# Kernel tuning notes

Measured on AMD Instinct MI355X. Metric: run time of the kernel, lower is better.

The kernel has to match this reference:

```python
import jax, jax.numpy as jnp
import numpy as np

NUM_TAGS = 32
START_ID = 29
STOP_ID = 30
PAD_ID = 31
VOCAB = 50000
EMB = 256
HID = 512          # bidirectional total; per-direction hidden = HID // 2
HD = HID // 2
B = 64
T = 512


def setup_inputs() -> dict:
    key = jax.random.key(0)
    ks = jax.random.split(key, 14)
    # pack_padded_sequence requires sorted-descending lengths; padding at the end
    lengths = np.sort(np.asarray(jax.random.randint(ks[0], (B,), T // 2, T + 1)))[::-1].copy()
    mask = (np.arange(T)[None, :] < lengths[:, None]).astype(np.int32)
    inp = jax.random.randint(ks[1], (B, T), 0, VOCAB, dtype=jnp.int32)
    gold = jax.random.randint(ks[2], (B, T), 0, START_ID, dtype=jnp.int32)  # real tags only
    s = 1.0 / np.sqrt(HD)
    emb = jax.random.normal(ks[3], (VOCAB, EMB), jnp.float32)
    Wih_f = jax.random.uniform(ks[4], (4 * HD, EMB), jnp.float32, -s, s)
    Whh_f = jax.random.uniform(ks[5], (4 * HD, HD), jnp.float32, -s, s)
    b_f = jax.random.uniform(ks[6], (4 * HD,), jnp.float32, -s, s)      # b_ih + b_hh combined
    Wih_b = jax.random.uniform(ks[7], (4 * HD, EMB), jnp.float32, -s, s)
    Whh_b = jax.random.uniform(ks[8], (4 * HD, HD), jnp.float32, -s, s)
    b_b = jax.random.uniform(ks[9], (4 * HD,), jnp.float32, -s, s)
    sl = 1.0 / np.sqrt(HID)
    W_tag = jax.random.uniform(ks[10], (NUM_TAGS, HID), jnp.float32, -sl, sl)
    b_tag = jax.random.uniform(ks[11], (NUM_TAGS,), jnp.float32, -sl, sl)
    trans = np.asarray(jax.random.normal(ks[12], (NUM_TAGS, NUM_TAGS), jnp.float32)).copy()
    # CRF.__init__ constraints
    trans[START_ID, :] = -10000.0
    trans[:, STOP_ID] = -10000.0
    trans[:, PAD_ID] = -10000.0
    trans[PAD_ID, :] = -10000.0
    trans[PAD_ID, STOP_ID] = 0.0
    trans[PAD_ID, PAD_ID] = 0.0
    return dict(inp=inp, gold=gold, mask=jnp.asarray(mask), emb=emb,
                Wih_f=Wih_f, Whh_f=Whh_f, b_f=b_f,
                Wih_b=Wih_b, Whh_b=Whh_b, b_b=b_b,
                W_tag=W_tag, b_tag=b_tag, trans=jnp.asarray(trans))


def _lstm_dir(xW, m, Whh):
    """xW: [T,B,4H] precomputed input projection + bias; m: [T,B,1] float mask; Whh: [4H,H].
    Masked state update replicates packed-sequence behavior (padding at sequence end)."""
    Bb, H = xW.shape[1], Whh.shape[1]

    def step(carry, xm):
        h, c = carry
        x_t, m_t = xm
        g = x_t + h @ Whh.T
        i, f, gg, o = jnp.split(g, 4, axis=-1)  # torch gate order i,f,g,o
        c_new = jax.nn.sigmoid(f) * c + jax.nn.sigmoid(i) * jnp.tanh(gg)
        h_new = jax.nn.sigmoid(o) * jnp.tanh(c_new)
        c = m_t * c_new + (1.0 - m_t) * c
        h = m_t * h_new + (1.0 - m_t) * h
        return (h, c), h

    init = (jnp.zeros((Bb, H), xW.dtype), jnp.zeros((Bb, H), xW.dtype))
    _, hs = jax.lax.scan(step, init, (xW, m))
    return hs  # [T,B,H]


def _forward(inp, gold, mask, emb, Wih_f, Whh_f, b_f, Wih_b, Whh_b, b_b, W_tag, b_tag, trans):
    maskf = mask.astype(jnp.float32)          # [B,T]
    x = emb[inp]                               # [B,T,E]
    xT = jnp.swapaxes(x, 0, 1)                 # [T,B,E]
    mT = maskf.T[:, :, None]                   # [T,B,1]
    h_f = _lstm_dir(xT @ Wih_f.T + b_f, mT, Whh_f)                 # forward direction
    h_b = _lstm_dir((xT @ Wih_b.T + b_b)[::-1], mT[::-1], Whh_b)[::-1]  # backward direction
    h = jnp.concatenate([h_f, h_b], axis=-1)   # [T,B,HID]
    h_tag = (h @ W_tag.T + b_tag) * mT         # masked emissions, [T,B,K]

    K = trans.shape[0]
    Bb = h_tag.shape[1]
    score0 = jnp.full((Bb, K), -10000.0, jnp.float32).at[:, STOP_ID].set(0.0)

    def crf_step(score, em):
        emit_t, m_t = em  # [B,K], [B,1]
        # logsumexp over previous tag j of score[b,j] + emit[b,i] + trans[i,j]
        s = jax.nn.logsumexp(score[:, None, :] + emit_t[:, :, None] + trans[None], axis=-1)
        return m_t * s + (1.0 - m_t) * score, None

    scoreZ, _ = jax.lax.scan(crf_step, score0, (h_tag, mT))
    Z = jax.nn.logsumexp(scoreZ + trans[STOP_ID], axis=-1)  # [B]

    # gold path score (vectorized version of CRF.score)
    h_bt = jnp.swapaxes(h_tag, 0, 1)                          # [B,T,K]
    emit = jnp.take_along_axis(h_bt[:, :-1, :], gold[:, 1:, None].astype(jnp.int32), axis=2)[..., 0]
    tr = trans[gold[:, 1:], gold[:, :-1]]                     # [B,T-1]
    gscore = jnp.sum((emit + tr) * maskf[:, :-1], axis=1)
    lengths = maskf.sum(1).astype(jnp.int32)
    last_tag = jnp.take_along_axis(gold, (lengths - 1)[:, None], axis=1)[:, 0]
    gscore = gscore + trans[STOP_ID, last_tag]
    return Z - gscore  # [B]


def reference(inp, gold, mask, emb, Wih_f, Whh_f, b_f, Wih_b, Whh_b, b_b, W_tag, b_tag, trans):
    return _forward(inp, gold, mask, emb, Wih_f, Whh_f, b_f, Wih_b, Whh_b, b_b, W_tag, b_tag, trans)
```

## Files before the change

### kernel.cpp

```cpp
#include <hip/hip_runtime.h>
#include <stdint.h>

#define T_LEN 512
#define NB 64
#define STOPID 30
#define PADID 31

typedef unsigned short u16;
typedef unsigned int u32;
typedef long long i64;
typedef short bf8 __attribute__((ext_vector_type(8)));
typedef float f32x4 __attribute__((ext_vector_type(4)));
typedef int v4i __attribute__((ext_vector_type(4)));

__device__ __forceinline__ float bf2f(u16 v){ return __uint_as_float(((u32)v) << 16); }
__device__ __forceinline__ u16 f2bf(float f){
  u32 u = __float_as_uint(f);
  return (u16)((u + 0x7FFFu + ((u >> 16) & 1u)) >> 16);
}
__device__ __forceinline__ float sigm(float x){
  return __builtin_amdgcn_rcpf(1.0f + __expf(-x));
}
__device__ __forceinline__ float tanhfast(float x){
  return 1.0f - 2.0f*__builtin_amdgcn_rcpf(1.0f + __expf(2.0f*x));
}
__device__ __forceinline__ v4i mk4(i64 a, i64 b){
  union { i64 q[2]; v4i v; } u; u.q[0]=a; u.q[1]=b; return u.v;
}

#define WSCALE 2032.0f
#define HSCALE 127.0f

extern "C" __global__ __launch_bounds__(256) void kg_emb(
    const int* __restrict__ inp, const float* __restrict__ emb,
    const int* __restrict__ mask,
    const float* __restrict__ whf, const float* __restrict__ whb,
    const float* __restrict__ wif, const float* __restrict__ wib,
    const float* __restrict__ wtag,
    u16* __restrict__ xemb, int* __restrict__ lenv,
    u32* __restrict__ whh8, u16* __restrict__ wih_bf, u16* __restrict__ wtag_bf)
{
  int r = blockIdx.x*2 + (threadIdx.x >> 7);
  int col = (threadIdx.x & 127) * 2;
  int b = r & 63, t = r >> 6;
  int tok = inp[b*T_LEN + t];
  float2 v = *(const float2*)(emb + (size_t)tok*256 + col);
  u32 pk = ((u32)f2bf(v.x)) | (((u32)f2bf(v.y)) << 16);
  *(u32*)(xemb + (size_t)r*256 + col) = pk;

  if (blockIdx.x < 1024) {
    int i = blockIdx.x * 256 + threadIdx.x;
    wih_bf[i]          = f2bf(wif[i]);
    wih_bf[262144 + i] = f2bf(wib[i]);
    if (i < 16384) wtag_bf[i] = f2bf(wtag[i]);
    if (i < 131072) {
      const float* src = (i < 65536) ? (whf + (size_t)i*4) : (whb + (size_t)(i - 65536)*4);
      float4 w4 = *(const float4*)src;
      int b0 = (int)rintf(fminf(fmaxf(w4.x*WSCALE, -127.f), 127.f));
      int b1 = (int)rintf(fminf(fmaxf(w4.y*WSCALE, -127.f), 127.f));
      int b2 = (int)rintf(fminf(fmaxf(w4.z*WSCALE, -127.f), 127.f));
      int b3 = (int)rintf(fminf(fmaxf(w4.w*WSCALE, -127.f), 127.f));
      whh8[i] = (u32)(b0 & 0xFF) | ((u32)(b1 & 0xFF) << 8)
              | ((u32)(b2 & 0xFF) << 16) | ((u32)(b3 & 0xFF) << 24);
    }
  }
  if (blockIdx.x == 0 && threadIdx.x < 64) {
    const int* mrow = mask + threadIdx.x * T_LEN;
    int lo = 256, hi = 512;
    while (lo < hi) { int mid = (lo + hi) >> 1; if (mrow[mid]) lo = mid + 1; else hi = mid; }
    lenv[threadIdx.x] = lo;
  }
}

extern "C" __global__ __launch_bounds__(256, 1) void k1_proj(
    const u16* __restrict__ xemb, const u16* __restrict__ wih,
    const float* __restrict__ b_f, const float* __restrict__ b_b,
    u16* __restrict__ xW)
{
  int tc = blockIdx.x;
  int gb = blockIdx.y;
  int dir  = gb >> 4;
  int nblk = gb & 15;
  int w    = threadIdx.x >> 6;
  int lane = threadIdx.x & 63;
  int lr = lane & 15, q = lane >> 4;

  bf8 bw[4][8];
  const u16* wbase = wih + (size_t)dir*262144 + (size_t)nblk*64*256;
  #pragma unroll
  for (int n = 0; n < 4; ++n)
    #pragma unroll
    for (int kt = 0; kt < 8; ++kt)
      bw[n][kt] = *(const bf8*)(wbase + (size_t)(n*16 + lr)*256 + kt*32 + q*8);
  #pragma unroll
  for (int n = 0; n < 4; ++n) {
    asm volatile("" : "+a"(bw[n][0]), "+a"(bw[n][1]), "+a"(bw[n][2]), "+a"(bw[n][3]));
    asm volatile("" : "+a"(bw[n][4]), "+a"(bw[n][5]), "+a"(bw[n][6]), "+a"(bw[n][7]));
  }

  const float* bias = dir ? b_b : b_f;
  float4 bv[4];
  #pragma unroll
  for (int n = 0; n < 4; ++n) bv[n] = *(const float4*)(bias + nblk*64 + n*16 + q*4);

  for (int ti = 0; ti < 8; ++ti) {
    int t = tc*8 + ti;
    bf8 af[8];
    #pragma unroll
    for (int kt = 0; kt < 8; ++kt)
      af[kt] = *(const bf8*)(xemb + ((size_t)t*64 + w*16 + lr)*256 + kt*32 + q*8);

    f32x4 acc[4];
    #pragma unroll
    for (int n = 0; n < 4; ++n) { acc[n][0]=0.f; acc[n][1]=0.f; acc[n][2]=0.f; acc[n][3]=0.f; }
    #pragma unroll
    for (int kt = 0; kt < 8; ++kt)
      #pragma unroll
      for (int n = 0; n < 4; ++n)
        acc[n] = __builtin_amdgcn_mfma_f32_16x16x32_bf16(bw[n][kt], af[kt], acc[n], 0, 0, 0);

    u16* xp = xW + ((size_t)(dir*4 + w)*T_LEN + t)*16384 + (size_t)lr*1024;
    #pragma unroll
    for (int n = 0; n < 4; ++n) {
      ushort4 st;
      st.x = f2bf(acc[n][0] + bv[n].x);
      st.y = f2bf(acc[n][1] + bv[n].y);
      st.z = f2bf(acc[n][2] + bv[n].z);
      st.w = f2bf(acc[n][3] + bv[n].w);
      *(ushort4*)(xp + nblk*64 + n*16 + q*4) = st;
    }
  }
}

extern "C" __global__ __launch_bounds__(512, 2) void k2_lstm(
    const u32* __restrict__ whh8, const u16* __restrict__ xW,
    const int* __restrict__ lenv, u16* __restrict__ h_out)
{
  __shared__ __align__(16) unsigned char hb[2][16*264];
  __shared__ __align__(16) int rd[8][2][4][36];

  int blk = blockIdx.x;
  int dir  = blk >> 5;
  int rgrp = blk & 31;
  int r0   = rgrp * 2;
  int rg16 = rgrp >> 3;
  int rb2  = (rgrp & 7) * 2;
  int w   = threadIdx.x >> 6;
  int lane = threadIdx.x & 63;
  int lr = lane & 15, q = lane >> 4;
  int cw = w * 32;
  int row = lr & 1;
  int hi  = lr >> 1;
  int chb = q*8 + hi;

  for (int i = threadIdx.x; i < 1056; i += 512)
    ((unsigned long long*)hb)[i] = 0ull;

  v4i bw[4][2][4];
  const unsigned char* wb = (const unsigned char*)whh8 + (size_t)dir*262144;
  #pragma unroll
  for (int g = 0; g < 4; ++g)
    #pragma unroll
    for (int s2 = 0; s2 < 2; ++s2)
      #pragma unroll
      for (int kt = 0; kt < 4; ++kt)
        bw[g][s2][kt] = *(const v4i*)(wb + (size_t)(g*256 + cw + 16*s2 + lr)*256 + kt*64 + q*16);
  #pragma unroll
  for (int g = 0; g < 4; ++g)
    #pragma unroll
    for (int s2 = 0; s2 < 2; ++s2)
      asm volatile("" : "+a"(bw[g][s2][0]), "+a"(bw[g][s2][1]), "+a"(bw[g][s2][2]), "+a"(bw[g][s2][3]));

  float cst = 0.f, hst = 0.f;
  int lnr = lenv[r0 + row];
  int* rdw = &rd[w][0][0][0];
  const float ginv = 1.0f/(WSCALE*HSCALE);

  int t0 = dir ? (T_LEN-1) : 0;
  int tstep = dir ? -1 : 1;
  i64 xstep  = (i64)tstep * 16384;
  i64 hostep = (i64)tstep * (NB*256);

  const u16* xp = xW + (size_t)(dir*4 + rg16)*T_LEN*16384
                     + (size_t)(rb2 + row)*1024 + cw + chb + (size_t)t0*16384;
  u16* ho = h_out + ((size_t)(dir*T_LEN + t0)*NB + r0 + row)*256 + cw + chb;
  int tcur = t0;

  u16 xc[4];
  #pragma unroll
  for (int g = 0; g < 4; ++g) xc[g] = xp[g*256];

  v4i z4; z4[0]=0; z4[1]=0; z4[2]=0; z4[3]=0;
  asm volatile("" : "+v"(z4));
  __syncthreads();

  for (int s = 0; s < T_LEN; ++s) {
    const unsigned char* hr = hb[s & 1];
    v4i afv[4];
    #pragma unroll
    for (int kt = 0; kt < 4; ++kt) {
      i64 lo = *(const i64*)(hr + lr*264 + kt*64 + q*16);
      i64 hi8 = *(const i64*)(hr + lr*264 + kt*64 + q*16 + 8);
      afv[kt] = mk4(lo, hi8);
    }

    v4i acc[2][4];
    #pragma unroll
    for (int s2 = 0; s2 < 2; ++s2)
      #pragma unroll
      for (int g = 0; g < 4; ++g)
        acc[s2][g] = __builtin_amdgcn_mfma_i32_16x16x64_i8(bw[g][s2][0], afv[0], z4, 0, 0, 0);
    #pragma unroll
    for (int kt = 1; kt < 4; ++kt)
      #pragma unroll
      for (int s2 = 0; s2 < 2; ++s2)
        #pragma unroll
        for (int g = 0; g < 4; ++g)
          acc[s2][g] = __builtin_amdgcn_mfma_i32_16x16x64_i8(bw[g][s2][kt], afv[kt], acc[s2][g], 0, 0, 0);

    if (lr < 2) {
      #pragma unroll
      for (int s2 = 0; s2 < 2; ++s2)
        #pragma unroll
        for (int g = 0; g < 4; ++g)
          *(v4i*)&rdw[(lr*4 + g)*36 + s2*16 + q*4] = acc[s2][g];
    }

    u16 xn[4];
    xp += xstep;
    if (s < T_LEN-1) {
      #pragma unroll
      for (int g = 0; g < 4; ++g) xn[g] = xp[g*256];
    } else {
      #pragma unroll
      for (int g = 0; g < 4; ++g) xn[g] = xc[g];
    }

    float gv[4];
    #pragma unroll
    for (int g = 0; g < 4; ++g)
      gv[g] = (float)rdw[(row*4 + g)*36 + chb] * ginv + bf2f(xc[g]);

    bool mk = (tcur < lnr);
    float cn = sigm(gv[1])*cst + sigm(gv[0])*tanhfast(gv[2]);
    float hn = sigm(gv[3])*tanhfast(cn);
    cst = mk ? cn : cst;
    hst = mk ? hn : hst;

    *ho = f2bf(hst);
    ho += hostep;
    tcur += tstep;

    int q0 = (int)rintf(hst*HSCALE);
    unsigned char* hw = hb[(s+1) & 1];
    hw[row*264 + cw + chb] = (unsigned char)(q0 & 0xFF);

    #pragma unroll
    for (int g = 0; g < 4; ++g) xc[g] = xn[g];

    asm volatile("s_waitcnt lgkmcnt(0)\n\ts_barrier" ::: "memory");
  }
}

extern "C" __global__ __launch_bounds__(256, 2) void k3_emit(
    const u16* __restrict__ h_out, const u16* __restrict__ wtag_bf,
    const float* __restrict__ b_tag, float* __restrict__ em)
{
  int wv = threadIdx.x >> 6, lane = threadIdx.x & 63;
  int lr = lane & 15, q = lane >> 4;
  size_t r0 = ((size_t)blockIdx.x*4 + wv) * 16;

  bf8 a[16];
  #pragma unroll
  for (int kt = 0; kt < 16; ++kt) {
    const u16* hp = h_out + (size_t)(kt>>3)*T_LEN*NB*256 + (r0 + lr)*256 + (kt&7)*32 + q*8;
    a[kt] = *(const bf8*)hp;
  }
  f32x4 acc[2];
  acc[0][0]=0.f;acc[0][1]=0.f;acc[0][2]=0.f;acc[0][3]=0.f; acc[1]=acc[0];
  #pragma unroll
  for (int n = 0; n < 2; ++n) {
    #pragma unroll
    for (int kt = 0; kt < 16; ++kt) {
      bf8 bfr = *(const bf8*)(wtag_bf + (size_t)(n*16 + lr)*512 + kt*32 + q*8);
      acc[n] = __builtin_amdgcn_mfma_f32_16x16x32_bf16(a[kt], bfr, acc[n], 0, 0, 0);
    }
  }
  #pragma unroll
  for (int n = 0; n < 2; ++n) {
    float bt = b_tag[n*16 + lr];
    #pragma unroll
    for (int J = 0; J < 4; ++J)
      em[(r0 + q*4 + J)*32 + n*16 + lr] = acc[n][J] + bt;
  }
}

extern "C" __global__ __launch_bounds__(64) void k5_crf(
    const int* __restrict__ gold, const int* __restrict__ lenv,
    const float* __restrict__ em, const float* __restrict__ trans,
    float* __restrict__ out)
{
  __shared__ float trans_s[32][33];
  int tid = threadIdx.x;
  for (int i = tid; i < 1024; i += 64) trans_s[i>>5][i&31] = trans[i];
  __syncthreads();

  int j = tid & 31;
  int hf = tid >> 5;
  int p0 = hf * 16;
  int b = blockIdx.x;
  int len = lenv[b];
  float score = (j == STOPID) ? 0.f : -10000.f;
  float gscore = 0.f;
  int g_cur = gold[b*T_LEN];

  float tr16[16], w16[16];
  #pragma unroll
  for (int pp = 0; pp < 16; ++pp) {
    tr16[pp] = trans_s[j][p0 + pp];
    w16[pp] = __expf(tr16[pp]);
  }

  float e = em[(size_t)b*32 + j];
  {
    float sv[16]; float mj = -3.0e38f;
    #pragma unroll
    for (int pp = 0; pp < 16; ++pp) {
      float sp = __shfl(score, p0 + pp, 32);
      sv[pp] = sp + tr16[pp];
      mj = fmaxf(mj, sv[pp]);
    }
    mj = fmaxf(mj, __shfl_xor(mj, 32));
    float se = 0.f;
    #pragma unroll
    for (int pp = 0; pp < 16; ++pp) se += __expf(sv[pp] - mj);
    se += __shfl_xor(se, 32);
    float ns = e + mj + __logf(se);
    int g_next = gold[b*T_LEN + 1];
    float emg = __shfl(e, g_next, 32);
    gscore += emg + trans_s[g_next][g_cur];
    g_cur = g_next;
    score = ns;
  }
  float m;
  {
    float mc = (j == PADID) ? -3.0e38f : score;
    #pragma unroll
    for (int off = 16; off; off >>= 1) mc = fmaxf(mc, __shfl_xor(mc, off, 32));
    m = mc;
  }
  e = em[((size_t)64 + b)*32 + j];
  for (int t = 1; t < len; ++t) {
    float en = (t+1 < len) ? em[((size_t)(t+1)*64 + b)*32 + j] : 0.f;
    float E = (j == PADID) ? 0.f : __expf(score - m);
    float s0 = 0.f, s1 = 0.f, s2 = 0.f, s3 = 0.f;
    #pragma unroll
    for (int pp = 0; pp < 16; pp += 4) {
      s0 += __shfl(E, p0 + pp + 0, 32) * w16[pp + 0];
      s1 += __shfl(E, p0 + pp + 1, 32) * w16[pp + 1];
      s2 += __shfl(E, p0 + pp + 2, 32) * w16[pp + 2];
      s3 += __shfl(E, p0 + pp + 3, 32) * w16[pp + 3];
    }
    float S = (s0 + s1) + (s2 + s3);
    S += __shfl_xor(S, 32);
    float ns = e + m + __logf(fmaxf(S, 1e-37f));
    if (j == PADID) ns = score + e;
    score = ns;
    if (t + 1 < T_LEN) {
      int g_next = gold[b*T_LEN + t + 1];
      float emg = __shfl(e, g_next, 32);
      gscore += emg + trans_s[g_next][g_cur];
      g_cur = g_next;
    }
    e = en;
    if (t & 1) {
      float mc = (j == PADID) ? -3.0e38f : score;
      #pragma unroll
      for (int off = 16; off; off >>= 1) mc = fmaxf(mc, __shfl_xor(mc, off, 32));
      m = mc;
    }
  }
  float v = score + trans_s[STOPID][j];
  float m2 = v;
  #pragma unroll
  for (int off = 16; off; off >>= 1) m2 = fmaxf(m2, __shfl_xor(m2, off, 32));
  float se2 = __expf(v - m2);
  #pragma unroll
  for (int off = 16; off; off >>= 1) se2 += __shfl_xor(se2, off, 32);
  float Z = m2 + __logf(se2);
  if (tid == 0) {
    int g_last = gold[b*T_LEN + len - 1];
    out[b] = Z - (gscore + trans_s[STOPID][g_last]);
  }
}

extern "C" void kernel_launch(void* const* d_in, const int* in_sizes, int n_in,
                              void* d_out, int out_size, void* d_ws, size_t ws_size,
                              hipStream_t stream)
{
  const int*   inp   = (const int*)  d_in[0];
  const int*   gold  = (const int*)  d_in[1];
  const int*   mask  = (const int*)  d_in[2];
  const float* emb   = (const float*)d_in[3];
  const float* Wih_f = (const float*)d_in[4];
  const float* Whh_f = (const float*)d_in[5];
  const float* b_f   = (const float*)d_in[6];
  const float* Wih_b = (const float*)d_in[7];
  const float* Whh_b = (const float*)d_in[8];
  const float* b_b   = (const float*)d_in[9];
  const float* W_tag = (const float*)d_in[10];
  const float* b_tag = (const float*)d_in[11];
  const float* trans = (const float*)d_in[12];
  float* out = (float*)d_out;

  char* ws = (char*)d_ws;
  u32* whh8   = (u32*)(ws + 0);
  u16* wtag_bf= (u16*)(ws + 524288);
  u16* wih_bf = (u16*)(ws + 1048576);
  u16* xW     = (u16*)(ws + 2097152);
  float* em   = (float*)(ws + 2097152);
  u16* h_outp = (u16*)(ws + 136314880);
  u16* xemb   = (u16*)(ws + 136314880);
  int* lenv   = (int*)(ws + 169869312);

  hipLaunchKernelGGL(kg_emb,  dim3(16384),    dim3(256), 0, stream,
                     inp, emb, mask, Whh_f, Whh_b, Wih_f, Wih_b, W_tag,
                     xemb, lenv, whh8, wih_bf, wtag_bf);
  hipLaunchKernelGGL(k1_proj, dim3(64, 32),   dim3(256), 0, stream,
                     xemb, wih_bf, b_f, b_b, xW);
  hipLaunchKernelGGL(k2_lstm, dim3(64),       dim3(512), 0, stream,
                     whh8, xW, lenv, h_outp);
  hipLaunchKernelGGL(k3_emit, dim3(512),      dim3(256), 0, stream,
                     h_outp, wtag_bf, b_tag, em);
  hipLaunchKernelGGL(k5_crf,  dim3(64),       dim3(64),  0, stream,
                     gold, lenv, em, trans, out);
}
```

Measured before the change: 1.042 ms.

## Stage gold tags in LDS, prefetch gold-path terms, use readfirstlane stabilizer

Copies each sequence's gold tags into shared memory and prefetches the gold-path emission and transition values two steps ahead, taking global loads and shuffles off the serial CRF recurrence. Replaces the periodic wave-wide max reduction used as the logsumexp stabilizer with a readfirstlane of lane 0's score. This shortens each time step's dependency chain. The cost is a less tight stabilizer, which could raise overflow or underflow risk when lane 0's score is far from the max.

```diff
diff --git a/kernel.cpp b/kernel.cpp
--- a/kernel.cpp
+++ b/kernel.cpp
@@ -301,18 +301,19 @@
     float* __restrict__ out)
 {
   __shared__ float trans_s[32][33];
+  __shared__ int gold_s[T_LEN];
   int tid = threadIdx.x;
+  int b = blockIdx.x;
   for (int i = tid; i < 1024; i += 64) trans_s[i>>5][i&31] = trans[i];
+  for (int i = tid; i < T_LEN; i += 64) gold_s[i] = gold[b*T_LEN + i];
   __syncthreads();
 
   int j = tid & 31;
   int hf = tid >> 5;
   int p0 = hf * 16;
-  int b = blockIdx.x;
   int len = lenv[b];
   float score = (j == STOPID) ? 0.f : -10000.f;
   float gscore = 0.f;
-  int g_cur = gold[b*T_LEN];
 
   float tr16[16], w16[16];
   #pragma unroll
@@ -335,23 +336,28 @@
     #pragma unroll
     for (int pp = 0; pp < 16; ++pp) se += __expf(sv[pp] - mj);
     se += __shfl_xor(se, 32);
-    float ns = e + mj + __logf(se);
-    int g_next = gold[b*T_LEN + 1];
-    float emg = __shfl(e, g_next, 32);
-    gscore += emg + trans_s[g_next][g_cur];
-    g_cur = g_next;
-    score = ns;
-  }
-  float m;
-  {
-    float mc = (j == PADID) ? -3.0e38f : score;
-    #pragma unroll
-    for (int off = 16; off; off >>= 1) mc = fmaxf(mc, __shfl_xor(mc, off, 32));
-    m = mc;
-  }
+    score = e + mj + __logf(se);
+  }
+  int g0 = gold_s[0], g1 = gold_s[1];
+  gscore += em[(size_t)b*32 + g1] + trans_s[g1][g0];
+
+  float m = __uint_as_float(__builtin_amdgcn_readfirstlane(__float_as_uint(score)));
+
+  int g_cur  = g1;
+  int g_next = gold_s[2];
+  int g_nn   = gold_s[3];
+  float emg_cur = em[((size_t)64 + b)*32 + g_next];
+  float tr_cur  = trans_s[g_next][g_cur];
   e = em[((size_t)64 + b)*32 + j];
+
   for (int t = 1; t < len; ++t) {
+    int t1 = (t+1 < T_LEN) ? (t+1) : (T_LEN-1);
+    int i3 = (t+3 < T_LEN) ? (t+3) : (T_LEN-1);
+    int g_nnn = gold_s[i3];
     float en = (t+1 < len) ? em[((size_t)(t+1)*64 + b)*32 + j] : 0.f;
+    float emg_next = em[((size_t)t1*64 + b)*32 + g_nn];
+    float tr_next  = trans_s[g_nn][g_next];
+
     float E = (j == PADID) ? 0.f : __expf(score - m);
     float s0 = 0.f, s1 = 0.f, s2 = 0.f, s3 = 0.f;
     #pragma unroll
@@ -366,19 +372,13 @@
     float ns = e + m + __logf(fmaxf(S, 1e-37f));
     if (j == PADID) ns = score + e;
     score = ns;
-    if (t + 1 < T_LEN) {
-      int g_next = gold[b*T_LEN + t + 1];
-      float emg = __shfl(e, g_next, 32);
-      gscore += emg + trans_s[g_next][g_cur];
-      g_cur = g_next;
-    }
+    m = __uint_as_float(__builtin_amdgcn_readfirstlane(__float_as_uint(score)));
+
+    if (t < T_LEN-1) gscore += emg_cur + tr_cur;
+
+    g_cur = g_next; g_next = g_nn; g_nn = g_nnn;
+    emg_cur = emg_next; tr_cur = tr_next;
     e = en;
-    if (t & 1) {
-      float mc = (j == PADID) ? -3.0e38f : score;
-      #pragma unroll
-      for (int off = 16; off; off >>= 1) mc = fmaxf(mc, __shfl_xor(mc, off, 32));
-      m = mc;
-    }
   }
   float v = score + trans_s[STOPID][j];
   float m2 = v;
@@ -389,7 +389,7 @@
   for (int off = 16; off; off >>= 1) se2 += __shfl_xor(se2, off, 32);
   float Z = m2 + __logf(se2);
   if (tid == 0) {
-    int g_last = gold[b*T_LEN + len - 1];
+    int g_last = gold_s[len - 1];
     out[b] = Z - (gscore + trans_s[STOPID][g_last]);
   }
 }
```

New measurement: 1.046 ms. No clear change (+0.3%).
